# Kernel tuning notes

Measured on AMD Instinct MI355X. Metric: run time of the kernel, lower is better.

## Reference

```python
import jax, jax.numpy as jnp
import numpy as np

NUM_HEADS = 16
HEAD_DIM = 64
D_MODEL = NUM_HEADS * HEAD_DIM


def setup_inputs() -> dict:
    key = jax.random.key(0)
    ks = jax.random.split(key, 7)
    B, S = 2, 2048
    q = jax.random.normal(ks[0], (B, S, D_MODEL), dtype=jnp.float32)
    k = jax.random.normal(ks[1], (B, S, D_MODEL), dtype=jnp.float32)
    v = jax.random.normal(ks[2], (B, S, D_MODEL), dtype=jnp.float32)
    scale = 1.0 / np.sqrt(D_MODEL).astype(np.float32)
    w_q = jax.random.normal(ks[3], (D_MODEL, D_MODEL), dtype=jnp.float32) * scale
    w_k = jax.random.normal(ks[4], (D_MODEL, D_MODEL), dtype=jnp.float32) * scale
    w_v = jax.random.normal(ks[5], (D_MODEL, D_MODEL), dtype=jnp.float32) * scale
    w_o = jax.random.normal(ks[6], (D_MODEL, D_MODEL), dtype=jnp.float32) * scale
    return {"q": q, "k": k, "v": v, "w_q": w_q, "w_k": w_k, "w_v": w_v, "w_o": w_o}


def reference(q, k, v, w_q, w_k, w_v, w_o):
    B, S, _ = q.shape
    H, D = NUM_HEADS, HEAD_DIM
    # projections; q scaled by 1/sqrt(dim) as in the original (dim = per-head dim)
    qh = (q @ w_q) / jnp.sqrt(jnp.asarray(D, q.dtype))
    kh = k @ w_k
    vh = v @ w_v
    # tf.split(axis=-1) into H chunks == reshape [B,S,H,D]
    qh = qh.reshape(B, S, H, D)
    kh = kh.reshape(B, S, H, D)
    vh = vh.reshape(B, S, H, D)
    # keras Attention: scores = q @ k^T, softmax over keys, @ v (no extra scale)
    scores = jnp.einsum("bqhd,bkhd->bhqk", qh, kh)
    probs = jax.nn.softmax(scores, axis=-1)
    o = jnp.einsum("bhqk,bkhd->bqhd", probs, vh)
    o = o.reshape(B, S, H * D)
    return o @ w_o
```

## Files before the change

### kernel.cpp

```cpp
#include <hip/hip_runtime.h>
#include <hip/hip_bf16.h>


using bf16x8 = __attribute__((ext_vector_type(8))) short;
using f32x4  = __attribute__((ext_vector_type(4))) float;
using u32x4  = __attribute__((ext_vector_type(4))) unsigned;
typedef unsigned short u16;
using u16x4 = __attribute__((ext_vector_type(4))) u16;
using u16x8 = __attribute__((ext_vector_type(8))) u16;

#define GLDS16(g, l) __builtin_amdgcn_global_load_lds( \
    (const __attribute__((address_space(1))) void*)(g), \
    (__attribute__((address_space(3))) void*)(l), 16, 0, 0)

#if __has_builtin(__builtin_amdgcn_exp2f)
#define EXP2(x) __builtin_amdgcn_exp2f(x)
#else
#define EXP2(x) exp2f(x)
#endif

__device__ __forceinline__ void block_sync() {
  __builtin_amdgcn_sched_barrier(0);
  asm volatile("" ::: "memory");
  __builtin_amdgcn_s_barrier();
  asm volatile("" ::: "memory");
  __builtin_amdgcn_sched_barrier(0);
}

__device__ __forceinline__ u16 f2bf(float f) {
  unsigned u = __builtin_bit_cast(unsigned, f);
  u += 0x7fffu + ((u >> 16) & 1u);
  return (u16)(u >> 16);
}

__device__ __forceinline__ unsigned cvt_pk_bf16(float lo, float hi) {
  unsigned r;
  asm("v_cvt_pk_bf16_f32 %0, %1, %2" : "=v"(r) : "v"(lo), "v"(hi));
  return r;
}

__device__ __forceinline__ float fmax3(float a, float b, float c) {
  return fmaxf(fmaxf(a, b), c);
}

__global__ __launch_bounds__(256) void wtrans_kernel(
    const float* __restrict__ wq, const float* __restrict__ wk,
    const float* __restrict__ wv, const float* __restrict__ wo,
    u16* __restrict__ dst) {
  __shared__ float t[32][33];
  const int z = blockIdx.z;
  const float* src = (z == 0) ? wq : (z == 1) ? wk : (z == 2) ? wv : wo;
  u16* d = dst + (size_t)z * 1024 * 1024;
  const int tx = threadIdx.x & 31, ty = threadIdx.x >> 5;
  const int bx = blockIdx.x * 32, by = blockIdx.y * 32;
#pragma unroll
  for (int j = 0; j < 4; j++)
    t[ty + j * 8][tx] = src[(size_t)(by + ty + j * 8) * 1024 + bx + tx];
  __syncthreads();
#pragma unroll
  for (int j = 0; j < 4; j++)
    d[(size_t)(bx + ty + j * 8) * 1024 + by + tx] = f2bf(t[tx][ty + j * 8]);
}

__global__ __launch_bounds__(256) void proj_kernel(
    const float* __restrict__ qf, const float* __restrict__ kf,
    const float* __restrict__ vf, const u16* __restrict__ WT,
    u16* __restrict__ Qh, u16* __restrict__ Kh, u16* __restrict__ Vt) {
  __shared__ u16 lds[16384];
  u16* ldsA = lds;
  u16* ldsB = lds + 8192;
  const int id = blockIdx.x;
  const int xcd = id & 7, l = id >> 3;
  const int z = l >> 5, rem = l & 31;
  const int by = xcd * 4 + (rem >> 3);
  const int bx = rem & 7;
  const int arow0 = by * 128, bcol0 = bx * 128;
  const float* A = (z == 0) ? qf : (z == 1) ? kf : vf;
  const u16* Bw = WT + (size_t)z * 1024 * 1024;

  const int tid = threadIdx.x;
  const int lane = tid & 63, wave = tid >> 6;
  const int lr = lane & 15, lg = lane >> 4;
  const int wr = (wave >> 1) * 64, wc = (wave & 1) * 64;
  f32x4 acc[4][4] = {};

  for (int kt = 0; kt < 1024; kt += 64) {
#pragma unroll
    for (int i = 0; i < 4; i++) {
      int o = (i * 256 + tid) * 8;
      int row = o >> 6, ch = (o >> 3) & 7;
      int sc = (ch ^ (row & 7)) << 3;
      GLDS16(Bw + (size_t)(bcol0 + row) * 1024 + kt + sc, &ldsB[o]);
    }
#pragma unroll
    for (int i = 0; i < 4; i++) {
      int o = (i * 256 + tid) * 8;
      int row = o >> 6, ch = (o >> 3) & 7;
      const float* ap = A + (size_t)(arow0 + row) * 1024 + kt + ch * 8;
      float4 f0 = *(const float4*)ap;
      float4 f1 = *(const float4*)(ap + 4);
      u32x4 w = {cvt_pk_bf16(f0.x, f0.y), cvt_pk_bf16(f0.z, f0.w),
                 cvt_pk_bf16(f1.x, f1.y), cvt_pk_bf16(f1.z, f1.w)};
      *(u32x4*)&ldsA[row * 64 + ((ch ^ (row & 7)) << 3)] = w;
    }
    __syncthreads();
#pragma unroll
    for (int kk = 0; kk < 2; kk++) {
      bf16x8 af[4], bfr[4];
      const int ke = kk * 32 + lg * 8;
#pragma unroll
      for (int m = 0; m < 4; m++) {
        int row = wr + m * 16 + lr;
        af[m] = *(const bf16x8*)&ldsA[row * 64 + (ke ^ ((row & 7) << 3))];
      }
#pragma unroll
      for (int n = 0; n < 4; n++) {
        int row = wc + n * 16 + lr;
        bfr[n] = *(const bf16x8*)&ldsB[row * 64 + (ke ^ ((row & 7) << 3))];
      }
#pragma unroll
      for (int m = 0; m < 4; m++)
#pragma unroll
        for (int n = 0; n < 4; n++)
          acc[m][n] = __builtin_amdgcn_mfma_f32_16x16x32_bf16(af[m], bfr[n],
                                                              acc[m][n], 0, 0, 0);
    }
    __syncthreads();
  }

  if (z == 2) {
    u16* T = lds;
#pragma unroll
    for (int m = 0; m < 4; m++)
#pragma unroll
      for (int n = 0; n < 4; n++)
#pragma unroll
        for (int r = 0; r < 4; r++) {
          int sl = wr + m * 16 + lg * 4 + r;
          int cl = wc + n * 16 + lr;
          T[cl * 128 + (sl ^ ((cl & 7) << 3))] = f2bf(acc[m][n][r]);
        }
    __syncthreads();
    const int t = threadIdx.x;
    const int cl = t >> 1, s0 = (t & 1) * 64;
    const int gc = bcol0 + cl;
    const size_t vrow = ((size_t)(arow0 >> 11) * 16 + (gc >> 6)) * 64 + (gc & 63);
#pragma unroll
    for (int j = 0; j < 8; j++) {
      int sl = s0 + j * 8;
      u16x8 vv = *(const u16x8*)&T[cl * 128 + (sl ^ ((cl & 7) << 3))];
      *(u16x8*)&Vt[vrow * 2048 + (size_t)((arow0 & 2047) + sl)] = vv;
    }
  } else {
    const float scale = (z == 0) ? 0.18033688f : 1.0f;
    u16* dst = (z == 0) ? Qh : Kh;
#pragma unroll
    for (int m = 0; m < 4; m++)
#pragma unroll
      for (int n = 0; n < 4; n++)
#pragma unroll
        for (int r = 0; r < 4; r++) {
          int gr = arow0 + wr + m * 16 + lg * 4 + r;
          int gc = bcol0 + wc + n * 16 + lr;
          size_t idx = (((size_t)(gr >> 11) * 16 + (gc >> 6)) * 2048 +
                        (gr & 2047)) * 64 + (gc & 63);
          dst[idx] = f2bf(acc[m][n][r] * scale);
        }
  }
}

__global__ __launch_bounds__(512, 4) void attn_kernel(
    const u16* __restrict__ Qh, const u16* __restrict__ Kh,
    const u16* __restrict__ Vt, u16* __restrict__ Ob) {
  __shared__ u16 kt[4][64 * 64];
  __shared__ u16 vt[4][64 * 64];
  const int tid = threadIdx.x;
  const int lane = tid & 63, wave = tid >> 6;
  const int lr = lane & 15, lg = lane >> 4;
  const int id = blockIdx.x;
  const int swz = (id & 7) * 64 + (id >> 3);
  const int bh = swz >> 4;
  const int q0 = (swz & 15) * 128;
  const u16* Qb = Qh + ((size_t)bh * 2048 + q0) * 64;
  const u16* Kb = Kh + (size_t)bh * 2048 * 64;
  const u16* Vb = Vt + (size_t)bh * 64 * 2048;

  bf16x8 aq[2];
#pragma unroll
  for (int kk = 0; kk < 2; kk++)
    aq[kk] = *(const bf16x8*)(Qb + (wave * 16 + lr) * 64 + kk * 32 + lg * 8);

  const int hsw = (lr & 3) | (((lr >> 2) & 1) << 2);
  int koff[2][4];
#pragma unroll
  for (int n = 0; n < 4; n++) {
    int kr = 32 * (n >> 1) + 8 * (lr >> 2) + 4 * (n & 1) + (lr & 3);
#pragma unroll
    for (int kk = 0; kk < 2; kk++)
      koff[kk][n] = kr * 64 + ((kk * 32 + lg * 8) ^ (hsw << 3));
  }
  int voff[2][4];
#pragma unroll
  for (int n = 0; n < 4; n++) {
    int d = n * 16 + lr;
#pragma unroll
    for (int ks = 0; ks < 2; ks++)
      voff[ks][n] = d * 64 + ((ks * 32 + lg * 8) ^ ((d & 7) << 3));
  }

  const int o0 = tid * 8;
  const int srow = tid >> 3, sch = tid & 7;
  const int hk = (srow & 3) | (((srow >> 3) & 1) << 2);
  const u16* kg = Kb + (size_t)srow * 64 + ((sch ^ hk) << 3);
  const u16* vg = Vb + (size_t)srow * 2048 + ((sch ^ (srow & 7)) << 3);

  f32x4 oacc[4] = {};
  float mrun = -1e30f, lrun = 0.f;

  auto STAGE = [&](int t, int b) {
    GLDS16(kg + (size_t)t * 4096, &kt[0][0] + b * 4096 + o0);
    GLDS16(vg + t * 64, &vt[0][0] + b * 4096 + o0);
  };

  auto COMPUTE = [&](int cur) {
    f32x4 sacc[4] = {};
    __builtin_amdgcn_s_setprio(1);
#pragma unroll
    for (int kk = 0; kk < 2; kk++) {
#pragma unroll
      for (int n = 0; n < 4; n++) {
        bf16x8 ka = *(const bf16x8*)&kt[cur][koff[kk][n]];
        sacc[n] = __builtin_amdgcn_mfma_f32_16x16x32_bf16(ka, aq[kk],
                                                          sacc[n], 0, 0, 0);
      }
    }
    __builtin_amdgcn_s_setprio(0);
    float t0 = fmax3(sacc[0][0], sacc[0][1], sacc[0][2]);
    float t1 = fmax3(sacc[0][3], sacc[1][0], sacc[1][1]);
    float t2 = fmax3(sacc[1][2], sacc[1][3], sacc[2][0]);
    float t3 = fmax3(sacc[2][1], sacc[2][2], sacc[2][3]);
    float t4 = fmax3(sacc[3][0], sacc[3][1], sacc[3][2]);
    float mx = fmaxf(fmax3(t0, t1, t2), fmax3(t3, t4, sacc[3][3]));
    mx = fmaxf(mx, __shfl_xor(mx, 16));
    mx = fmaxf(mx, __shfl_xor(mx, 32));
    float mnew = fmaxf(mrun, mx);
    if (__all(mx - mrun <= 8.0f)) {
      mnew = mrun;
    } else {
      float corr = EXP2(mrun - mnew);
      mrun = mnew;
      lrun *= corr;
      float cr[4];
#pragma unroll
      for (int r = 0; r < 4; r++) cr[r] = __shfl(corr, lg * 4 + r);
#pragma unroll
      for (int n = 0; n < 4; n++)
#pragma unroll
        for (int r = 0; r < 4; r++) oacc[n][r] *= cr[r];
    }
    float psum = 0.f;
#pragma unroll
    for (int n = 0; n < 4; n++)
#pragma unroll
      for (int r = 0; r < 4; r++) {
        float p = EXP2(sacc[n][r] - mnew);
        sacc[n][r] = p;
        psum += p;
      }
    psum += __shfl_xor(psum, 16);
    psum += __shfl_xor(psum, 32);
    lrun += psum;
    u32x4 w0 = {cvt_pk_bf16(sacc[0][0], sacc[0][1]),
                cvt_pk_bf16(sacc[0][2], sacc[0][3]),
                cvt_pk_bf16(sacc[1][0], sacc[1][1]),
                cvt_pk_bf16(sacc[1][2], sacc[1][3])};
    u32x4 w1 = {cvt_pk_bf16(sacc[2][0], sacc[2][1]),
                cvt_pk_bf16(sacc[2][2], sacc[2][3]),
                cvt_pk_bf16(sacc[3][0], sacc[3][1]),
                cvt_pk_bf16(sacc[3][2], sacc[3][3])};
    bf16x8 pa0 = __builtin_bit_cast(bf16x8, w0);
    bf16x8 pa1 = __builtin_bit_cast(bf16x8, w1);
    __builtin_amdgcn_s_setprio(1);
#pragma unroll
    for (int ks = 0; ks < 2; ks++) {
      bf16x8 ap = ks ? pa1 : pa0;
      bf16x8 bv[4];
#pragma unroll
      for (int n = 0; n < 4; n++)
        bv[n] = *(const bf16x8*)&vt[cur][voff[ks][n]];
#pragma unroll
      for (int n = 0; n < 4; n++)
        oacc[n] = __builtin_amdgcn_mfma_f32_16x16x32_bf16(ap, bv[n],
                                                          oacc[n], 0, 0, 0);
    }
    __builtin_amdgcn_s_setprio(0);
  };

#define VMC6 asm volatile("s_waitcnt vmcnt(6)" ::: "memory")
#define VMC4 asm volatile("s_waitcnt vmcnt(4)" ::: "memory")
#define VMC2 asm volatile("s_waitcnt vmcnt(2)" ::: "memory")
#define VMC0 asm volatile("s_waitcnt vmcnt(0)" ::: "memory")
  STAGE(0, 0); STAGE(1, 1); STAGE(2, 2);
  for (int t = 0; t < 28; t += 4) {
    STAGE(t + 3, 3); VMC6; block_sync(); COMPUTE(0); block_sync();
    STAGE(t + 4, 0); VMC6; block_sync(); COMPUTE(1); block_sync();
    STAGE(t + 5, 1); VMC6; block_sync(); COMPUTE(2); block_sync();
    STAGE(t + 6, 2); VMC6; block_sync(); COMPUTE(3); block_sync();
  }
  STAGE(31, 3); VMC6; block_sync(); COMPUTE(0); block_sync();
  VMC4; block_sync(); COMPUTE(1); block_sync();
  VMC2; block_sync(); COMPUTE(2); block_sync();
  VMC0; block_sync(); COMPUTE(3);
#undef VMC6
#undef VMC4
#undef VMC2
#undef VMC0

  const int b = bh >> 4, h = bh & 15;
  float inv = 1.0f / lrun;
  float ivr[4];
#pragma unroll
  for (int r = 0; r < 4; r++) ivr[r] = __shfl(inv, lg * 4 + r);
#pragma unroll
  for (int r = 0; r < 4; r++) {
    int qrow = q0 + wave * 16 + lg * 4 + r;
#pragma unroll
    for (int n = 0; n < 4; n++) {
      int d = n * 16 + lr;
      Ob[((size_t)b * 2048 + qrow) * 1024 + h * 64 + d] = f2bf(oacc[n][r] * ivr[r]);
    }
  }
}

__global__ __launch_bounds__(256) void outproj_kernel(
    const u16* __restrict__ Ob, const u16* __restrict__ WoT,
    float* __restrict__ out) {
  __shared__ u16 ldsA[128 * 64];
  __shared__ u16 ldsB[64 * 64];
  const int tid = threadIdx.x;
  const int lane = tid & 63, wave = tid >> 6;
  const int lr = lane & 15, lg = lane >> 4;
  const int wr = (wave >> 1) * 64;
  const int wc = (wave & 1) * 32;
  const int id = blockIdx.x;
  const int xcd = id & 7, l = id >> 3;
  const int by = xcd * 4 + (l >> 4);
  const int bx = l & 15;
  const int arow0 = by * 128, bcol0 = bx * 64;
  f32x4 acc[4][2] = {};
  for (int kt = 0; kt < 1024; kt += 64) {
#pragma unroll
    for (int i = 0; i < 4; i++) {
      int o = (i * 256 + tid) * 8;
      int row = o >> 6, ch = (o >> 3) & 7;
      int sc = (ch ^ (row & 7)) << 3;
      GLDS16(Ob + (size_t)(arow0 + row) * 1024 + kt + sc, &ldsA[o]);
    }
#pragma unroll
    for (int i = 0; i < 2; i++) {
      int o = (i * 256 + tid) * 8;
      int row = o >> 6, ch = (o >> 3) & 7;
      int sc = (ch ^ (row & 7)) << 3;
      GLDS16(WoT + (size_t)(bcol0 + row) * 1024 + kt + sc, &ldsB[o]);
    }
    __syncthreads();
#pragma unroll
    for (int kk = 0; kk < 2; kk++) {
      const int ke = kk * 32 + lg * 8;
      bf16x8 af[4], bfr[2];
#pragma unroll
      for (int m = 0; m < 4; m++) {
        int row = wr + m * 16 + lr;
        af[m] = *(const bf16x8*)&ldsA[row * 64 + (ke ^ ((row & 7) << 3))];
      }
#pragma unroll
      for (int n = 0; n < 2; n++) {
        int row = wc + n * 16 + lr;
        bfr[n] = *(const bf16x8*)&ldsB[row * 64 + (ke ^ ((row & 7) << 3))];
      }
#pragma unroll
      for (int m = 0; m < 4; m++)
#pragma unroll
        for (int n = 0; n < 2; n++)
          acc[m][n] = __builtin_amdgcn_mfma_f32_16x16x32_bf16(af[m], bfr[n],
                                                              acc[m][n], 0, 0, 0);
    }
    __syncthreads();
  }
#pragma unroll
  for (int m = 0; m < 4; m++)
#pragma unroll
    for (int n = 0; n < 2; n++)
#pragma unroll
      for (int r = 0; r < 4; r++) {
        int gr = arow0 + wr + m * 16 + lg * 4 + r;
        int gc = bcol0 + wc + n * 16 + lr;
        out[(size_t)gr * 1024 + gc] = acc[m][n][r];
      }
}

extern "C" void kernel_launch(void* const* d_in, const int* in_sizes, int n_in,
                              void* d_out, int out_size, void* d_ws, size_t ws_size,
                              hipStream_t stream) {
  const float* q  = (const float*)d_in[0];
  const float* k  = (const float*)d_in[1];
  const float* v  = (const float*)d_in[2];
  const float* wq = (const float*)d_in[3];
  const float* wk = (const float*)d_in[4];
  const float* wv = (const float*)d_in[5];
  const float* wo = (const float*)d_in[6];
  float* out = (float*)d_out;
  char* ws = (char*)d_ws;

  u16* WT = (u16*)ws;
  u16* Qh = (u16*)(ws + (size_t)32 * 1024 * 1024);
  u16* Kh = (u16*)(ws + (size_t)40 * 1024 * 1024);
  u16* Vt = (u16*)(ws + (size_t)48 * 1024 * 1024);
  u16* Ob = (u16*)(ws + (size_t)56 * 1024 * 1024);

  wtrans_kernel<<<dim3(32, 32, 4), 256, 0, stream>>>(wq, wk, wv, wo, WT);
  proj_kernel<<<dim3(768), 256, 0, stream>>>(q, k, v, WT, Qh, Kh, Vt);
  attn_kernel<<<dim3(512), 512, 0, stream>>>(Qh, Kh, Vt, Ob);
  outproj_kernel<<<dim3(512), 256, 0, stream>>>(Ob, WT + (size_t)3 * 1024 * 1024, out);
}
```

Baseline: 128.5 us.

## Software-pipeline projection GEMM: prefetch next A tile to registers, double-buffer B

Restructures the projection GEMM main loop so the next k-tile's fp32 A data is loaded into registers and the next B tile is fetched into a second LDS buffer while MFMAs run on the current tile. Uses explicit vmcnt waits and barriers in place of the prior load-then-sync scheme, and sets the launch bound to 3 blocks per CU. This targets global-load latency that was previously exposed each iteration. In exchange it uses more LDS (48KB) and more registers for the prefetched A, which may lower occupancy, and the hand-written waitcnt counts must match the issued loads to stay correct.

After: 121.6 us. 1.06x faster.

```diff
diff --git a/kernel.cpp b/kernel.cpp
--- a/kernel.cpp
+++ b/kernel.cpp
@@ -62,13 +62,11 @@
     d[(size_t)(bx + ty + j * 8) * 1024 + by + tx] = f2bf(t[tx][ty + j * 8]);
 }
 
-__global__ __launch_bounds__(256) void proj_kernel(
+__global__ __launch_bounds__(256, 3) void proj_kernel(
     const float* __restrict__ qf, const float* __restrict__ kf,
     const float* __restrict__ vf, const u16* __restrict__ WT,
     u16* __restrict__ Qh, u16* __restrict__ Kh, u16* __restrict__ Vt) {
-  __shared__ u16 lds[16384];
-  u16* ldsA = lds;
-  u16* ldsB = lds + 8192;
+  __shared__ u16 lds[24576];
   const int id = blockIdx.x;
   const int xcd = id & 7, l = id >> 3;
   const int z = l >> 5, rem = l & 31;
@@ -82,28 +80,49 @@
   const int lane = tid & 63, wave = tid >> 6;
   const int lr = lane & 15, lg = lane >> 4;
   const int wr = (wave >> 1) * 64, wc = (wave & 1) * 64;
+  const int ar = tid >> 3, ac = tid & 7;
   f32x4 acc[4][4] = {};
 
-  for (int kt = 0; kt < 1024; kt += 64) {
+  f32x4 fa[4][2];
+  u32x4 w[4];
+
+  auto LOADA = [&](int kt) {
+#pragma unroll
+    for (int i = 0; i < 4; i++) {
+      const float* ap = A + (size_t)(arow0 + i * 32 + ar) * 1024 + kt + ac * 8;
+      fa[i][0] = *(const f32x4*)ap;
+      fa[i][1] = *(const f32x4*)(ap + 4);
+    }
+  };
+  auto GLDSB = [&](int kt, int nb) {
+    u16* bd = lds + 8192 + nb * 8192;
 #pragma unroll
     for (int i = 0; i < 4; i++) {
       int o = (i * 256 + tid) * 8;
       int row = o >> 6, ch = (o >> 3) & 7;
       int sc = (ch ^ (row & 7)) << 3;
-      GLDS16(Bw + (size_t)(bcol0 + row) * 1024 + kt + sc, &ldsB[o]);
-    }
+      GLDS16(Bw + (size_t)(bcol0 + row) * 1024 + kt + sc, bd + o);
+    }
+  };
+  auto CVT = [&]() {
 #pragma unroll
     for (int i = 0; i < 4; i++) {
-      int o = (i * 256 + tid) * 8;
-      int row = o >> 6, ch = (o >> 3) & 7;
-      const float* ap = A + (size_t)(arow0 + row) * 1024 + kt + ch * 8;
-      float4 f0 = *(const float4*)ap;
-      float4 f1 = *(const float4*)(ap + 4);
-      u32x4 w = {cvt_pk_bf16(f0.x, f0.y), cvt_pk_bf16(f0.z, f0.w),
-                 cvt_pk_bf16(f1.x, f1.y), cvt_pk_bf16(f1.z, f1.w)};
-      *(u32x4*)&ldsA[row * 64 + ((ch ^ (row & 7)) << 3)] = w;
-    }
-    __syncthreads();
+      u32x4 v = {cvt_pk_bf16(fa[i][0][0], fa[i][0][1]),
+                 cvt_pk_bf16(fa[i][0][2], fa[i][0][3]),
+                 cvt_pk_bf16(fa[i][1][0], fa[i][1][1]),
+                 cvt_pk_bf16(fa[i][1][2], fa[i][1][3])};
+      w[i] = v;
+    }
+  };
+  auto WRITEA = [&]() {
+#pragma unroll
+    for (int i = 0; i < 4; i++) {
+      int row = i * 32 + ar;
+      *(u32x4*)&lds[row * 64 + ((ac ^ (row & 7)) << 3)] = w[i];
+    }
+  };
+  auto MFMAK = [&](int cb) {
+    const u16* Bb = lds + 8192 + cb * 8192;
 #pragma unroll
     for (int kk = 0; kk < 2; kk++) {
       bf16x8 af[4], bfr[4];
@@ -111,12 +130,12 @@
 #pragma unroll
       for (int m = 0; m < 4; m++) {
         int row = wr + m * 16 + lr;
-        af[m] = *(const bf16x8*)&ldsA[row * 64 + (ke ^ ((row & 7) << 3))];
+        af[m] = *(const bf16x8*)&lds[row * 64 + (ke ^ ((row & 7) << 3))];
       }
 #pragma unroll
       for (int n = 0; n < 4; n++) {
         int row = wc + n * 16 + lr;
-        bfr[n] = *(const bf16x8*)&ldsB[row * 64 + (ke ^ ((row & 7) << 3))];
+        bfr[n] = *(const bf16x8*)&Bb[row * 64 + (ke ^ ((row & 7) << 3))];
       }
 #pragma unroll
       for (int m = 0; m < 4; m++)
@@ -125,11 +144,35 @@
           acc[m][n] = __builtin_amdgcn_mfma_f32_16x16x32_bf16(af[m], bfr[n],
                                                               acc[m][n], 0, 0, 0);
     }
-    __syncthreads();
-  }
+  };
+
+#define PSTEP(KT, CB, MORE)                                                  \
+  do {                                                                       \
+    CVT();                                                                   \
+    if (MORE) { LOADA((KT) + 64); GLDSB((KT) + 64, (CB) ^ 1); }              \
+    WRITEA();                                                                \
+    if (MORE)                                                                \
+      asm volatile("s_waitcnt vmcnt(12) lgkmcnt(0)" ::: "memory");           \
+    else                                                                     \
+      asm volatile("s_waitcnt vmcnt(0) lgkmcnt(0)" ::: "memory");            \
+    block_sync();                                                            \
+    MFMAK(CB);                                                               \
+    block_sync();                                                            \
+  } while (0)
+
+  LOADA(0);
+  GLDSB(0, 0);
+  for (int kt = 0; kt < 896; kt += 128) {
+    PSTEP(kt, 0, true);
+    PSTEP(kt + 64, 1, true);
+  }
+  PSTEP(896, 0, true);
+  PSTEP(960, 1, false);
+#undef PSTEP
 
   if (z == 2) {
     u16* T = lds;
+    __syncthreads();
 #pragma unroll
     for (int m = 0; m < 4; m++)
 #pragma unroll
```

## Shrink projection tiles to 64x64 and software-pipeline A/B loads

Applied to the files above, without the earlier changes.

The QKV projection kernel moves from 128x128 tiles (768 blocks) to 64x64 tiles (3072 blocks) and sets a higher occupancy hint. Its k-loop is now software-pipelined: the fp32 A tile is prefetched into registers and the B tile is double-buffered in LDS, with explicit waitcnt so the next loads overlap the current MFMAs. Q/K outputs are staged through LDS so each thread does vectorized 16-byte global stores instead of scattered 2-byte writes. Smaller tiles give more parallelism and latency hiding across the CUs, at the cost of less operand reuse per block and more total global traffic.

New measurement: 133.6 us. 1.04x slower.

```diff
diff --git a/kernel.cpp b/kernel.cpp
--- a/kernel.cpp
+++ b/kernel.cpp
@@ -5,8 +5,8 @@
 using bf16x8 = __attribute__((ext_vector_type(8))) short;
 using f32x4  = __attribute__((ext_vector_type(4))) float;
 using u32x4  = __attribute__((ext_vector_type(4))) unsigned;
+using u32x2  = __attribute__((ext_vector_type(2))) unsigned;
 typedef unsigned short u16;
-using u16x4 = __attribute__((ext_vector_type(4))) u16;
 using u16x8 = __attribute__((ext_vector_type(8))) u16;
 
 #define GLDS16(g, l) __builtin_amdgcn_global_load_lds( \
@@ -62,110 +62,147 @@
     d[(size_t)(bx + ty + j * 8) * 1024 + by + tx] = f2bf(t[tx][ty + j * 8]);
 }
 
-__global__ __launch_bounds__(256) void proj_kernel(
+__global__ __launch_bounds__(256, 6) void proj_kernel(
     const float* __restrict__ qf, const float* __restrict__ kf,
     const float* __restrict__ vf, const u16* __restrict__ WT,
     u16* __restrict__ Qh, u16* __restrict__ Kh, u16* __restrict__ Vt) {
-  __shared__ u16 lds[16384];
-  u16* ldsA = lds;
-  u16* ldsB = lds + 8192;
+  __shared__ u16 lds[12288];
   const int id = blockIdx.x;
-  const int xcd = id & 7, l = id >> 3;
-  const int z = l >> 5, rem = l & 31;
-  const int by = xcd * 4 + (rem >> 3);
-  const int bx = rem & 7;
-  const int arow0 = by * 128, bcol0 = bx * 128;
+  const int xcd = id & 7, r0 = id >> 3;
+  const int z = r0 >> 7, rem = r0 & 127;
+  const int yp = xcd * 8 + (rem >> 4);
+  const int bx = rem & 15;
+  const int arow0 = yp * 64, bcol0 = bx * 64;
   const float* A = (z == 0) ? qf : (z == 1) ? kf : vf;
   const u16* Bw = WT + (size_t)z * 1024 * 1024;
 
   const int tid = threadIdx.x;
   const int lane = tid & 63, wave = tid >> 6;
   const int lr = lane & 15, lg = lane >> 4;
-  const int wr = (wave >> 1) * 64, wc = (wave & 1) * 64;
-  f32x4 acc[4][4] = {};
-
-  for (int kt = 0; kt < 1024; kt += 64) {
-#pragma unroll
-    for (int i = 0; i < 4; i++) {
+  const int wr = (wave >> 1) * 32, wc = (wave & 1) * 32;
+  const int ar = tid >> 2, ac0 = (tid & 3) * 16;
+  f32x4 acc[2][2] = {};
+  f32x4 fa[4];
+
+  auto LOADA = [&](int kt) {
+    const float* ap = A + (size_t)(arow0 + ar) * 1024 + kt + ac0;
+#pragma unroll
+    for (int j = 0; j < 4; j++) fa[j] = *(const f32x4*)(ap + 4 * j);
+  };
+  auto GLDSB = [&](int kt, int nb) {
+    u16* bd = lds + 4096 + nb * 4096;
+#pragma unroll
+    for (int i = 0; i < 2; i++) {
       int o = (i * 256 + tid) * 8;
       int row = o >> 6, ch = (o >> 3) & 7;
-      int sc = (ch ^ (row & 7)) << 3;
-      GLDS16(Bw + (size_t)(bcol0 + row) * 1024 + kt + sc, &ldsB[o]);
-    }
-#pragma unroll
-    for (int i = 0; i < 4; i++) {
-      int o = (i * 256 + tid) * 8;
-      int row = o >> 6, ch = (o >> 3) & 7;
-      const float* ap = A + (size_t)(arow0 + row) * 1024 + kt + ch * 8;
-      float4 f0 = *(const float4*)ap;
-      float4 f1 = *(const float4*)(ap + 4);
-      u32x4 w = {cvt_pk_bf16(f0.x, f0.y), cvt_pk_bf16(f0.z, f0.w),
-                 cvt_pk_bf16(f1.x, f1.y), cvt_pk_bf16(f1.z, f1.w)};
-      *(u32x4*)&ldsA[row * 64 + ((ch ^ (row & 7)) << 3)] = w;
-    }
-    __syncthreads();
+      GLDS16(Bw + (size_t)(bcol0 + row) * 1024 + kt + ((ch ^ (row & 7)) << 3),
+             bd + o);
+    }
+  };
+  auto WRITEA = [&]() {
+    u32x2 c0 = {cvt_pk_bf16(fa[0][0], fa[0][1]), cvt_pk_bf16(fa[0][2], fa[0][3])};
+    u32x2 c1 = {cvt_pk_bf16(fa[1][0], fa[1][1]), cvt_pk_bf16(fa[1][2], fa[1][3])};
+    u32x2 c2 = {cvt_pk_bf16(fa[2][0], fa[2][1]), cvt_pk_bf16(fa[2][2], fa[2][3])};
+    u32x2 c3 = {cvt_pk_bf16(fa[3][0], fa[3][1]), cvt_pk_bf16(fa[3][2], fa[3][3])};
+    u32x4 lo = {c0[0], c0[1], c1[0], c1[1]};
+    u32x4 hi = {c2[0], c2[1], c3[0], c3[1]};
+    const int swz = (ar & 7) << 3;
+    *(u32x4*)&lds[ar * 64 + (ac0 ^ swz)] = lo;
+    *(u32x4*)&lds[ar * 64 + ((ac0 + 8) ^ swz)] = hi;
+  };
+  auto MFMAK = [&](int cb) {
+    const u16* Bb = lds + 4096 + cb * 4096;
 #pragma unroll
     for (int kk = 0; kk < 2; kk++) {
-      bf16x8 af[4], bfr[4];
       const int ke = kk * 32 + lg * 8;
-#pragma unroll
-      for (int m = 0; m < 4; m++) {
+      bf16x8 af[2], bfr[2];
+#pragma unroll
+      for (int m = 0; m < 2; m++) {
         int row = wr + m * 16 + lr;
-        af[m] = *(const bf16x8*)&ldsA[row * 64 + (ke ^ ((row & 7) << 3))];
-      }
-#pragma unroll
-      for (int n = 0; n < 4; n++) {
+        af[m] = *(const bf16x8*)&lds[row * 64 + (ke ^ ((row & 7) << 3))];
+      }
+#pragma unroll
+      for (int n = 0; n < 2; n++) {
         int row = wc + n * 16 + lr;
-        bfr[n] = *(const bf16x8*)&ldsB[row * 64 + (ke ^ ((row & 7) << 3))];
-      }
-#pragma unroll
-      for (int m = 0; m < 4; m++)
-#pragma unroll
-        for (int n = 0; n < 4; n++)
+        bfr[n] = *(const bf16x8*)&Bb[row * 64 + (ke ^ ((row & 7) << 3))];
+      }
+#pragma unroll
+      for (int m = 0; m < 2; m++)
+#pragma unroll
+        for (int n = 0; n < 2; n++)
           acc[m][n] = __builtin_amdgcn_mfma_f32_16x16x32_bf16(af[m], bfr[n],
                                                               acc[m][n], 0, 0, 0);
     }
-    __syncthreads();
-  }
-
+  };
+
+#define STEPF(KT, CB)                                                        \
+  do {                                                                       \
+    asm volatile("s_waitcnt vmcnt(2)" ::: "memory");        \
+    WRITEA();                           \
+    LOADA((KT) + 64);                                                        \
+    GLDSB((KT) + 64, (CB) ^ 1);                                              \
+    asm volatile("s_waitcnt vmcnt(6) lgkmcnt(0)" ::: "memory");    \
+    block_sync();                                                            \
+    MFMAK(CB);                                                               \
+    block_sync();                                                            \
+  } while (0)
+
+  LOADA(0);
+  GLDSB(0, 0);
+  for (int kt = 0; kt < 896; kt += 128) {
+    STEPF(kt, 0);
+    STEPF(kt + 64, 1);
+  }
+  STEPF(896, 0);
+  {
+    asm volatile("s_waitcnt vmcnt(2)" ::: "memory");
+    WRITEA();
+    asm volatile("s_waitcnt vmcnt(0) lgkmcnt(0)" ::: "memory");
+    block_sync();
+    MFMAK(1);
+    block_sync();
+  }
+#undef STEPF
+
+  const size_t bh = (size_t)(arow0 >> 11) * 16 + bx;
+  const int sbase = arow0 & 2047;
+  u16* T = lds;
   if (z == 2) {
-    u16* T = lds;
-#pragma unroll
-    for (int m = 0; m < 4; m++)
-#pragma unroll
-      for (int n = 0; n < 4; n++)
+#pragma unroll
+    for (int m = 0; m < 2; m++)
+#pragma unroll
+      for (int n = 0; n < 2; n++)
 #pragma unroll
         for (int r = 0; r < 4; r++) {
           int sl = wr + m * 16 + lg * 4 + r;
           int cl = wc + n * 16 + lr;
-          T[cl * 128 + (sl ^ ((cl & 7) << 3))] = f2bf(acc[m][n][r]);
+          T[cl * 64 + (sl ^ ((cl & 7) << 3))] = f2bf(acc[m][n][r]);
         }
     __syncthreads();
-    const int t = threadIdx.x;
-    const int cl = t >> 1, s0 = (t & 1) * 64;
-    const int gc = bcol0 + cl;
-    const size_t vrow = ((size_t)(arow0 >> 11) * 16 + (gc >> 6)) * 64 + (gc & 63);
-#pragma unroll
-    for (int j = 0; j < 8; j++) {
-      int sl = s0 + j * 8;
-      u16x8 vv = *(const u16x8*)&T[cl * 128 + (sl ^ ((cl & 7) << 3))];
-      *(u16x8*)&Vt[vrow * 2048 + (size_t)((arow0 & 2047) + sl)] = vv;
-    }
+    const int d = tid >> 2, s0 = (tid & 3) * 16;
+    const int swz = (d & 7) << 3;
+    u16* vd = Vt + (bh * 64 + d) * 2048 + sbase;
+    *(u16x8*)&vd[s0] = *(const u16x8*)&T[d * 64 + (s0 ^ swz)];
+    *(u16x8*)&vd[s0 + 8] = *(const u16x8*)&T[d * 64 + ((s0 + 8) ^ swz)];
   } else {
     const float scale = (z == 0) ? 0.18033688f : 1.0f;
     u16* dst = (z == 0) ? Qh : Kh;
 #pragma unroll
-    for (int m = 0; m < 4; m++)
-#pragma unroll
-      for (int n = 0; n < 4; n++)
+    for (int m = 0; m < 2; m++)
+#pragma unroll
+      for (int n = 0; n < 2; n++)
 #pragma unroll
         for (int r = 0; r < 4; r++) {
-          int gr = arow0 + wr + m * 16 + lg * 4 + r;
-          int gc = bcol0 + wc + n * 16 + lr;
-          size_t idx = (((size_t)(gr >> 11) * 16 + (gc >> 6)) * 2048 +
-                        (gr & 2047)) * 64 + (gc & 63);
-          dst[idx] = f2bf(acc[m][n][r] * scale);
+          int sl = wr + m * 16 + lg * 4 + r;
+          int cl = wc + n * 16 + lr;
+          T[sl * 64 + (cl ^ ((sl & 7) << 3))] = f2bf(acc[m][n][r] * scale);
         }
+    __syncthreads();
+    const int s = tid >> 2, c0 = (tid & 3) * 16;
+    const int swz = (s & 7) << 3;
+    u16* qd = dst + (bh * 2048 + (size_t)(sbase + s)) * 64;
+    *(u16x8*)&qd[c0] = *(const u16x8*)&T[s * 64 + (c0 ^ swz)];
+    *(u16x8*)&qd[c0 + 8] = *(const u16x8*)&T[s * 64 + ((c0 + 8) ^ swz)];
   }
 }
 
@@ -419,7 +456,7 @@
   u16* Ob = (u16*)(ws + (size_t)56 * 1024 * 1024);
 
   wtrans_kernel<<<dim3(32, 32, 4), 256, 0, stream>>>(wq, wk, wv, wo, WT);
-  proj_kernel<<<dim3(768), 256, 0, stream>>>(q, k, v, WT, Qh, Kh, Vt);
+  proj_kernel<<<dim3(3072), 256, 0, stream>>>(q, k, v, WT, Qh, Kh, Vt);
   attn_kernel<<<dim3(512), 512, 0, stream>>>(Qh, Kh, Vt, Ob);
   outproj_kernel<<<dim3(512), 256, 0, stream>>>(Ob, WT + (size_t)3 * 1024 * 1024, out);
 }
```
